# Performance work log

Measured on AMD Instinct MI355X. Metric: run time of the kernel, lower is better.

## Reference

```python
import jax, jax.numpy as jnp
import numpy as np

N, D = 32768, 1024

def setup_inputs() -> dict:
    key = jax.random.key(0)
    k1, k2, k3 = jax.random.split(key, 3)
    elg = jax.random.normal(k1, (N, D), dtype=jnp.float32)
    eth = jax.random.normal(k2, (N, D), dtype=jnp.float32)
    weight = jax.random.normal(k3, (D, D), dtype=jnp.float32)
    return {"elg": elg, "eth": eth, "weight": weight}

def reference(elg, eth, weight):
    # out[n] = elg[n] @ W @ eth[n]  -- batched bilinear form, fully fused
    return jnp.einsum('nd,de,ne->n', elg, weight, eth)
```

## Files before the change

kernel.cpp:

```cpp
#include <hip/hip_runtime.h>
#include <hip/hip_bf16.h>

typedef __attribute__((ext_vector_type(8))) short short8;
typedef __attribute__((ext_vector_type(4))) float float4v;
typedef __attribute__((ext_vector_type(4))) unsigned int uint4v;

#define DDIM 1024
#define M_TILE 64
#define ETH_STRIDE 1032

__device__ __forceinline__ unsigned short f2bf(float f) {
  unsigned u = __builtin_bit_cast(unsigned, f);
  unsigned r = (u + 0x7fffu + ((u >> 16) & 1u)) >> 16;
  return (unsigned short)r;
}
__device__ __forceinline__ unsigned pk2(float lo, float hi) {
  return (unsigned)f2bf(lo) | ((unsigned)f2bf(hi) << 16);
}

__global__ __launch_bounds__(256) void convert_w(const float* __restrict__ W,
                                                 unsigned short* __restrict__ Wb) {
  size_t i = ((size_t)blockIdx.x * 256 + threadIdx.x) * 8;
  float4v a = *(const float4v*)(W + i);
  float4v b = *(const float4v*)(W + i + 4);
  uint4v pk;
  pk.x = pk2(a.x, a.y); pk.y = pk2(a.z, a.w);
  pk.z = pk2(b.x, b.y); pk.w = pk2(b.z, b.w);
  *(uint4v*)(Wb + i) = pk;
}

__global__ __launch_bounds__(256) void bilinear_kernel(const float* __restrict__ elg,
                                                       const float* __restrict__ eth,
                                                       const unsigned short* __restrict__ Wb,
                                                       float* __restrict__ out) {
  __shared__ unsigned short ethL[M_TILE * ETH_STRIDE];
  __shared__ unsigned short Wbuf[256 * 32];
  __shared__ float wsum[4][64];

  const int tid  = threadIdx.x;
  const int lane = tid & 63;
  const int w    = tid >> 6;
  const int quad = lane >> 4;
  const int l15  = lane & 15;
  const int m0   = blockIdx.x * M_TILE;

  uint4v wreg[4];
  {
    const int rbase = tid >> 2, up = tid & 3;
#pragma unroll
    for (int i = 0; i < 4; ++i) {
      int r = rbase + 64 * i;
      int u = up ^ ((r >> 1) & 3);
      wreg[i] = *(const uint4v*)(Wb + (size_t)r * DDIM + u * 8);
    }
  }

#pragma unroll
  for (int it = 0; it < 32; ++it) {
    int g = tid + 256 * it;
    int row = g >> 7, cg = g & 127;
    const float* src = eth + (size_t)(m0 + row) * DDIM + cg * 8;
    float4v a = *(const float4v*)(src);
    float4v b = *(const float4v*)(src + 4);
    uint4v pk;
    pk.x = pk2(a.x, a.y); pk.y = pk2(a.z, a.w);
    pk.z = pk2(b.x, b.y); pk.w = pk2(b.z, b.w);
    *(uint4v*)&ethL[row * ETH_STRIDE + cg * 8] = pk;
  }

  float p[16];
#pragma unroll
  for (int j = 0; j < 16; ++j) p[j] = 0.f;

  for (int dIter = 0; dIter < 4; ++dIter) {
    const int d0 = dIter * 256;
    float4v acc[4][4];
#pragma unroll
    for (int ct = 0; ct < 4; ++ct)
#pragma unroll
      for (int rt = 0; rt < 4; ++rt)
        acc[ct][rt] = (float4v){0.f, 0.f, 0.f, 0.f};

    for (int ek = 0; ek < 32; ++ek) {
      __syncthreads();
#pragma unroll
      for (int i = 0; i < 4; ++i)
        *(uint4v*)&Wbuf[tid * 8 + i * 2048] = wreg[i];
      __syncthreads();

      int cN = dIter * 32 + ek + 1;
      if (cN < 128) {
        int d0n = (cN >> 5) * 256, e0n = (cN & 31) * 32;
        const int rbase = tid >> 2, up = tid & 3;
#pragma unroll
        for (int i = 0; i < 4; ++i) {
          int r = rbase + 64 * i;
          int u = up ^ ((r >> 1) & 3);
          wreg[i] = *(const uint4v*)(Wb + (size_t)(d0n + r) * DDIM + e0n + u * 8);
        }
      }

      short8 aF[4], bF[4];
#pragma unroll
      for (int rt = 0; rt < 4; ++rt)
        aF[rt] = *(const short8*)&ethL[(rt * 16 + l15) * ETH_STRIDE + ek * 32 + quad * 8];
#pragma unroll
      for (int ct = 0; ct < 4; ++ct) {
        int r = w * 64 + ct * 16 + l15;
        int pu = quad ^ ((r >> 1) & 3);
        bF[ct] = *(const short8*)&Wbuf[r * 32 + pu * 8];
      }
#pragma unroll
      for (int ct = 0; ct < 4; ++ct)
#pragma unroll
        for (int rt = 0; rt < 4; ++rt)
          acc[ct][rt] = __builtin_amdgcn_mfma_f32_16x16x32_bf16(aF[rt], bF[ct], acc[ct][rt], 0, 0, 0);
    }

#pragma unroll
    for (int ct = 0; ct < 4; ++ct) {
      int col = d0 + w * 64 + ct * 16 + l15;
#pragma unroll
      for (int rt = 0; rt < 4; ++rt) {
        const float* ep = elg + (size_t)(m0 + rt * 16 + quad * 4) * DDIM + col;
#pragma unroll
        for (int i = 0; i < 4; ++i)
          p[rt * 4 + i] += acc[ct][rt][i] * ep[(size_t)i * DDIM];
      }
    }
  }

#pragma unroll
  for (int off = 1; off < 16; off <<= 1)
#pragma unroll
    for (int j = 0; j < 16; ++j)
      p[j] += __shfl_xor(p[j], off);

  if (l15 == 0) {
#pragma unroll
    for (int rt = 0; rt < 4; ++rt)
#pragma unroll
      for (int i = 0; i < 4; ++i)
        wsum[w][rt * 16 + quad * 4 + i] = p[rt * 4 + i];
  }
  __syncthreads();
  if (tid < 64)
    out[m0 + tid] = wsum[0][tid] + wsum[1][tid] + wsum[2][tid] + wsum[3][tid];
}

extern "C" void kernel_launch(void* const* d_in, const int* in_sizes, int n_in,
                              void* d_out, int out_size, void* d_ws, size_t ws_size,
                              hipStream_t stream) {
  (void)in_sizes; (void)n_in; (void)out_size; (void)ws_size;
  const float* elg = (const float*)d_in[0];
  const float* eth = (const float*)d_in[1];
  const float* W   = (const float*)d_in[2];
  float* out = (float*)d_out;
  unsigned short* Wb = (unsigned short*)d_ws;

  convert_w<<<dim3(512), dim3(256), 0, stream>>>(W, Wb);
  bilinear_kernel<<<dim3(512), dim3(256), 0, stream>>>(elg, eth, Wb, out);
}
```

Baseline: 403.4 us.

## Split D across blocks with atomic reduction and stream eth tiles through small LDS

Each block now handles one 64-row tile and one 256-column slice of D, launching four times as many blocks and combining partial sums with atomicAdd into a zeroed output. Eth is streamed in 32-column chunks into a small LDS buffer instead of staging the whole 64x1024 row tile, which cuts LDS use and permits an occupancy hint of 3 blocks per CU. W tiles are loaded directly to LDS with global_load_lds instead of going through registers. The cost is that the eth tile is converted and reloaded once per D slice (four times total), plus the atomics and an extra memset.

```diff
diff --git a/kernel.cpp b/kernel.cpp
--- a/kernel.cpp
+++ b/kernel.cpp
@@ -6,8 +6,7 @@
 typedef __attribute__((ext_vector_type(4))) unsigned int uint4v;
 
 #define DDIM 1024
-#define M_TILE 64
-#define ETH_STRIDE 1032
+#define ETH_STRIDE 40
 
 __device__ __forceinline__ unsigned short f2bf(float f) {
   unsigned u = __builtin_bit_cast(unsigned, f);
@@ -29,11 +28,11 @@
   *(uint4v*)(Wb + i) = pk;
 }
 
-__global__ __launch_bounds__(256) void bilinear_kernel(const float* __restrict__ elg,
-                                                       const float* __restrict__ eth,
-                                                       const unsigned short* __restrict__ Wb,
-                                                       float* __restrict__ out) {
-  __shared__ unsigned short ethL[M_TILE * ETH_STRIDE];
+__global__ __launch_bounds__(256, 3) void bilinear_kernel(const float* __restrict__ elg,
+                                                          const float* __restrict__ eth,
+                                                          const unsigned short* __restrict__ Wb,
+                                                          float* __restrict__ out) {
+  __shared__ unsigned short ethL[64 * ETH_STRIDE];
   __shared__ unsigned short Wbuf[256 * 32];
   __shared__ float wsum[4][64];
 
@@ -42,91 +41,83 @@
   const int w    = tid >> 6;
   const int quad = lane >> 4;
   const int l15  = lane & 15;
-  const int m0   = blockIdx.x * M_TILE;
+  const int m0   = (blockIdx.x >> 2) * 64;
+  const int d0   = (blockIdx.x & 3) * 256;
 
-  uint4v wreg[4];
-  {
-    const int rbase = tid >> 2, up = tid & 3;
+  const int erow = tid >> 2, eunit = tid & 3;
+  const float* esrc = eth + (size_t)(m0 + erow) * DDIM + eunit * 8;
+
+  const int wr = lane >> 2, wu = lane & 3;
+
+  float4v er0 = *(const float4v*)(esrc);
+  float4v er1 = *(const float4v*)(esrc + 4);
+
+  float4v acc[4][4];
 #pragma unroll
-    for (int i = 0; i < 4; ++i) {
-      int r = rbase + 64 * i;
-      int u = up ^ ((r >> 1) & 3);
-      wreg[i] = *(const uint4v*)(Wb + (size_t)r * DDIM + u * 8);
+  for (int ct = 0; ct < 4; ++ct)
+#pragma unroll
+    for (int rt = 0; rt < 4; ++rt)
+      acc[ct][rt] = (float4v){0.f, 0.f, 0.f, 0.f};
+
+  for (int ek = 0; ek < 32; ++ek) {
+    const int e0 = ek * 32;
+    __syncthreads();
+
+    {
+      uint4v pk;
+      pk.x = pk2(er0.x, er0.y); pk.y = pk2(er0.z, er0.w);
+      pk.z = pk2(er1.x, er1.y); pk.w = pk2(er1.z, er1.w);
+      *(uint4v*)&ethL[erow * ETH_STRIDE + eunit * 8] = pk;
     }
-  }
 
 #pragma unroll
-  for (int it = 0; it < 32; ++it) {
-    int g = tid + 256 * it;
-    int row = g >> 7, cg = g & 127;
-    const float* src = eth + (size_t)(m0 + row) * DDIM + cg * 8;
-    float4v a = *(const float4v*)(src);
-    float4v b = *(const float4v*)(src + 4);
-    uint4v pk;
-    pk.x = pk2(a.x, a.y); pk.y = pk2(a.z, a.w);
-    pk.z = pk2(b.x, b.y); pk.w = pk2(b.z, b.w);
-    *(uint4v*)&ethL[row * ETH_STRIDE + cg * 8] = pk;
+    for (int j = 0; j < 4; ++j) {
+      int r  = (w * 4 + j) * 16 + wr;
+      int ug = wu ^ ((r >> 1) & 3);
+      const unsigned short* gp = Wb + (size_t)(d0 + r) * DDIM + e0 + ug * 8;
+      unsigned short* lp = &Wbuf[(w * 4 + j) * 512 + lane * 8];
+      __builtin_amdgcn_global_load_lds(
+          (const __attribute__((address_space(1))) unsigned int*)gp,
+          (__attribute__((address_space(3))) unsigned int*)lp, 16, 0, 0);
+    }
+    __syncthreads();
+
+    short8 aF[4], bF[4];
+#pragma unroll
+    for (int rt = 0; rt < 4; ++rt)
+      aF[rt] = *(const short8*)&ethL[(rt * 16 + l15) * ETH_STRIDE + quad * 8];
+#pragma unroll
+    for (int ct = 0; ct < 4; ++ct) {
+      int dl = w * 64 + ct * 16 + l15;
+      int pu = quad ^ ((dl >> 1) & 3);
+      bF[ct] = *(const short8*)&Wbuf[dl * 32 + pu * 8];
+    }
+
+    if (ek < 31) {
+      const float* s = esrc + (e0 + 32);
+      er0 = *(const float4v*)(s);
+      er1 = *(const float4v*)(s + 4);
+    }
+
+#pragma unroll
+    for (int ct = 0; ct < 4; ++ct)
+#pragma unroll
+      for (int rt = 0; rt < 4; ++rt)
+        acc[ct][rt] = __builtin_amdgcn_mfma_f32_16x16x32_bf16(aF[rt], bF[ct], acc[ct][rt], 0, 0, 0);
   }
 
   float p[16];
 #pragma unroll
   for (int j = 0; j < 16; ++j) p[j] = 0.f;
-
-  for (int dIter = 0; dIter < 4; ++dIter) {
-    const int d0 = dIter * 256;
-    float4v acc[4][4];
 #pragma unroll
-    for (int ct = 0; ct < 4; ++ct)
+  for (int ct = 0; ct < 4; ++ct) {
+    int col = d0 + w * 64 + ct * 16 + l15;
 #pragma unroll
-      for (int rt = 0; rt < 4; ++rt)
-        acc[ct][rt] = (float4v){0.f, 0.f, 0.f, 0.f};
-
-    for (int ek = 0; ek < 32; ++ek) {
-      __syncthreads();
+    for (int rt = 0; rt < 4; ++rt) {
+      const float* ep = elg + (size_t)(m0 + rt * 16 + quad * 4) * DDIM + col;
 #pragma unroll
       for (int i = 0; i < 4; ++i)
-        *(uint4v*)&Wbuf[tid * 8 + i * 2048] = wreg[i];
-      __syncthreads();
-
-      int cN = dIter * 32 + ek + 1;
-      if (cN < 128) {
-        int d0n = (cN >> 5) * 256, e0n = (cN & 31) * 32;
-        const int rbase = tid >> 2, up = tid & 3;
-#pragma unroll
-        for (int i = 0; i < 4; ++i) {
-          int r = rbase + 64 * i;
-          int u = up ^ ((r >> 1) & 3);
-          wreg[i] = *(const uint4v*)(Wb + (size_t)(d0n + r) * DDIM + e0n + u * 8);
-        }
-      }
-
-      short8 aF[4], bF[4];
-#pragma unroll
-      for (int rt = 0; rt < 4; ++rt)
-        aF[rt] = *(const short8*)&ethL[(rt * 16 + l15) * ETH_STRIDE + ek * 32 + quad * 8];
-#pragma unroll
-      for (int ct = 0; ct < 4; ++ct) {
-        int r = w * 64 + ct * 16 + l15;
-        int pu = quad ^ ((r >> 1) & 3);
-        bF[ct] = *(const short8*)&Wbuf[r * 32 + pu * 8];
-      }
-#pragma unroll
-      for (int ct = 0; ct < 4; ++ct)
-#pragma unroll
-        for (int rt = 0; rt < 4; ++rt)
-          acc[ct][rt] = __builtin_amdgcn_mfma_f32_16x16x32_bf16(aF[rt], bF[ct], acc[ct][rt], 0, 0, 0);
-    }
-
-#pragma unroll
-    for (int ct = 0; ct < 4; ++ct) {
-      int col = d0 + w * 64 + ct * 16 + l15;
-#pragma unroll
-      for (int rt = 0; rt < 4; ++rt) {
-        const float* ep = elg + (size_t)(m0 + rt * 16 + quad * 4) * DDIM + col;
-#pragma unroll
-        for (int i = 0; i < 4; ++i)
-          p[rt * 4 + i] += acc[ct][rt][i] * ep[(size_t)i * DDIM];
-      }
+        p[rt * 4 + i] += acc[ct][rt][i] * ep[(size_t)i * DDIM];
     }
   }
 
@@ -144,20 +135,23 @@
         wsum[w][rt * 16 + quad * 4 + i] = p[rt * 4 + i];
   }
   __syncthreads();
-  if (tid < 64)
-    out[m0 + tid] = wsum[0][tid] + wsum[1][tid] + wsum[2][tid] + wsum[3][tid];
+  if (tid < 64) {
+    float s = wsum[0][tid] + wsum[1][tid] + wsum[2][tid] + wsum[3][tid];
+    atomicAdd(&out[m0 + tid], s);
+  }
 }
 
 extern "C" void kernel_launch(void* const* d_in, const int* in_sizes, int n_in,
                               void* d_out, int out_size, void* d_ws, size_t ws_size,
                               hipStream_t stream) {
-  (void)in_sizes; (void)n_in; (void)out_size; (void)ws_size;
+  (void)in_sizes; (void)n_in; (void)ws_size;
   const float* elg = (const float*)d_in[0];
   const float* eth = (const float*)d_in[1];
   const float* W   = (const float*)d_in[2];
   float* out = (float*)d_out;
   unsigned short* Wb = (unsigned short*)d_ws;
 
+  hipMemsetAsync(d_out, 0, (size_t)out_size * sizeof(float), stream);
   convert_w<<<dim3(512), dim3(256), 0, stream>>>(W, Wb);
-  bilinear_kernel<<<dim3(512), dim3(256), 0, stream>>>(elg, eth, Wb, out);
+  bilinear_kernel<<<dim3(2048), dim3(256), 0, stream>>>(elg, eth, Wb, out);
 }
```

Measured after the change: 368.3 us. -8.7%, faster.
